# Optimization experiments

Measured on AMD Instinct MI355X. Metric: run time of the kernel, lower is better.

Reference implementation:

```python
import jax, jax.numpy as jnp
import numpy as np

N = 100000   # nodes
E = 1600000  # edges
F = 128      # num_features
H = 128      # hidden width
G = 64       # graphs in batch (target_size)
C = 10       # output_channels


def setup_inputs() -> dict:
    key = jax.random.key(0)
    ks = jax.random.split(key, 16)
    s = 0.05
    inp = {
        "x": jax.random.normal(ks[0], (N, F), jnp.float32),
        "edge_index": jax.random.randint(ks[1], (2, E), 0, N, jnp.int32),
        "batch": jnp.sort(jax.random.randint(ks[2], (N,), 0, G, jnp.int32)),
        "target_size": G,
        # GraphConv layer params: lin_rel (weight+bias) applied to aggregated
        # neighbors, lin_root (weight, no bias) applied to self features.
        "W1_rel": jax.random.normal(ks[3], (H, F), jnp.float32) * s,
        "b1_rel": jnp.zeros((H,), jnp.float32),
        "W1_root": jax.random.normal(ks[4], (H, F), jnp.float32) * s,
        "W2_rel": jax.random.normal(ks[5], (H, H), jnp.float32) * s,
        "b2_rel": jnp.zeros((H,), jnp.float32),
        "W2_root": jax.random.normal(ks[6], (H, H), jnp.float32) * s,
        "W3_rel": jax.random.normal(ks[7], (H, H), jnp.float32) * s,
        "b3_rel": jnp.zeros((H,), jnp.float32),
        "W3_root": jax.random.normal(ks[8], (H, H), jnp.float32) * s,
        "Wl1": jax.random.normal(ks[9], (64, H), jnp.float32) * s,
        "bl1": jnp.zeros((64,), jnp.float32),
        "Wl2": jax.random.normal(ks[10], (C, 64), jnp.float32) * s,
        "bl2": jnp.zeros((C,), jnp.float32),
    }
    return inp


def _graph_conv(x, src, dst, W_rel, b_rel, W_root):
    # PyG GraphConv (aggr='add'): out_i = W_rel @ sum_{j->i} x_j + b_rel + W_root @ x_i
    agg = jax.ops.segment_sum(x[src], dst, num_segments=N)  # [N, F_in]
    return agg @ W_rel.T + b_rel + x @ W_root.T


def reference(x, edge_index, batch, target_size,
              W1_rel, b1_rel, W1_root,
              W2_rel, b2_rel, W2_root,
              W3_rel, b3_rel, W3_root,
              Wl1, bl1, Wl2, bl2):
    src, dst = edge_index[0], edge_index[1]
    h = jax.nn.relu(_graph_conv(x, src, dst, W1_rel, b1_rel, W1_root))
    h = jax.nn.relu(_graph_conv(h, src, dst, W2_rel, b2_rel, W2_root))
    h = jax.nn.relu(_graph_conv(h, src, dst, W3_rel, b3_rel, W3_root))
    # global_mean_pool over graph ids
    sums = jax.ops.segment_sum(h, batch, num_segments=target_size)        # [G, H]
    cnts = jax.ops.segment_sum(jnp.ones((N, 1), h.dtype), batch,
                               num_segments=target_size)                  # [G, 1]
    pooled = sums / jnp.maximum(cnts, 1.0)
    h = jax.nn.relu(pooled @ Wl1.T + bl1)
    return jax.nn.log_softmax(h @ Wl2.T + bl2, axis=-1)
```

## Files before the change

### kernel.cpp

```cpp
#include <hip/hip_runtime.h>

#define N_NODES 100000
#define NPAD    100096
#define N_EDGES 1600000
#define FDIM 128
#define GDIM 64
#define CDIM 10

#define BSH   9
#define BSIZE 512
#define NB    196
#define EPB   8192
#define EPB_C 6250

typedef unsigned short us16;
typedef us16 usx4 __attribute__((ext_vector_type(4)));
typedef us16 usx8 __attribute__((ext_vector_type(8)));
typedef short bfrag __attribute__((ext_vector_type(8)));
typedef float f32x4 __attribute__((ext_vector_type(4)));

__device__ __forceinline__ float bf2f(us16 u) {
  return __uint_as_float(((unsigned)u) << 16);
}
__device__ __forceinline__ us16 f2bf(float f) {
  unsigned u = __float_as_uint(f);
  u += 0x7FFFu + ((u >> 16) & 1u);
  return (us16)(u >> 16);
}

#define XB 6250
__global__ __launch_bounds__(256) void k_prep(
    const float* __restrict__ x, us16* __restrict__ xb,
    const float* __restrict__ Wrel1, const float* __restrict__ Wroot1,
    const float* __restrict__ Wrel2, const float* __restrict__ Wroot2,
    const float* __restrict__ Wrel3, const float* __restrict__ Wroot3,
    us16* __restrict__ Wp, float* __restrict__ pooled,
    const int* __restrict__ edst, int* __restrict__ bcnt) {
  int bx = blockIdx.x, tid = threadIdx.x;
  if (bx < XB) {
    size_t i = ((size_t)bx * 256 + tid) * 8;
    float4 a = *(const float4*)(x + i);
    float4 b = *(const float4*)(x + i + 4);
    usx8 o;
    o[0]=f2bf(a.x); o[1]=f2bf(a.y); o[2]=f2bf(a.z); o[3]=f2bf(a.w);
    o[4]=f2bf(b.x); o[5]=f2bf(b.y); o[6]=f2bf(b.z); o[7]=f2bf(b.w);
    *(usx8*)(xb + i) = o;
  } else if (bx < XB + 384) {
    int wb = bx - XB;
    int l = wb >> 7;
    const float* Wrel  = (l == 0) ? Wrel1  : (l == 1) ? Wrel2  : Wrel3;
    const float* Wroot = (l == 0) ? Wroot1 : (l == 1) ? Wroot2 : Wroot3;
    int idx = (wb & 127) * 256 + tid;
    int k = idx >> 7;
    int c = idx & 127;
    float v = (k < 128) ? Wrel[c * 128 + k] : Wroot[c * 128 + k - 128];
    Wp[(size_t)l * 32768 + (((k >> 3) * 128 + c) << 3) + (k & 7)] = f2bf(v);
  } else if (bx == XB + 384) {
    for (int i = tid; i < GDIM * FDIM; i += 256) pooled[i] = 0.f;
  } else {
    __shared__ int h[NB];
    int cb = bx - (XB + 385);
    for (int i = tid; i < NB; i += 256) h[i] = 0;
    __syncthreads();
    int s0 = cb * EPB;
    int e0 = s0 + EPB; if (e0 > N_EDGES) e0 = N_EDGES;
    for (int i = s0 + tid; i < e0; i += 256) atomicAdd(&h[edst[i] >> BSH], 1);
    __syncthreads();
    for (int i = tid; i < NB; i += 256)
      if (h[i]) atomicAdd(&bcnt[i], h[i]);
  }
}

__device__ __forceinline__ void scan_bcnt(const int* __restrict__ bcnt,
                                          int* wsum ,
                                          int* boffL , int tid) {
  int v = (tid < NB) ? bcnt[tid] : 0;
  int lane = tid & 63;
  int x = v;
#pragma unroll
  for (int d = 1; d < 64; d <<= 1) {
    int t = __shfl_up(x, d, 64);
    if (lane >= d) x += t;
  }
  if (tid < 256 && lane == 63) wsum[tid >> 6] = x;
  __syncthreads();
  if (tid == 0) {
    int r = 0;
#pragma unroll
    for (int i = 0; i < 4; ++i) { int t = wsum[i]; wsum[i] = r; r += t; }
  }
  __syncthreads();
  if (tid < NB) boffL[tid] = x - v + wsum[tid >> 6];
  __syncthreads();
}

__global__ __launch_bounds__(1024) void k_bscatter(
    const int* __restrict__ src, const int* __restrict__ dst,
    const int* __restrict__ bcnt, int* __restrict__ bcursor,
    int* __restrict__ ebuf) {
  __shared__ int wsum[4];
  __shared__ int boffL[NB];
  __shared__ int h[NB];
  __shared__ int base[NB];
  __shared__ int lc[NB];
  int tid = threadIdx.x;
  for (int i = tid; i < NB; i += 1024) h[i] = 0;
  scan_bcnt(bcnt, wsum, boffL, tid);
  int s0 = blockIdx.x * EPB_C;
  int e0 = s0 + EPB_C; if (e0 > N_EDGES) e0 = N_EDGES;
  for (int i = s0 + tid; i < e0; i += 1024) atomicAdd(&h[dst[i] >> BSH], 1);
  __syncthreads();
  for (int i = tid; i < NB; i += 1024) {
    base[i] = h[i] ? (boffL[i] + atomicAdd(&bcursor[i], h[i])) : 0;
    lc[i] = 0;
  }
  __syncthreads();
  for (int i = s0 + tid; i < e0; i += 1024) {
    int d = dst[i];
    int b = d >> BSH;
    int lp = atomicAdd(&lc[b], 1);
    ebuf[base[b] + lp] = (src[i] << BSH) | (d & (BSIZE - 1));
  }
}

__global__ __launch_bounds__(1024) void k_bucket_csr(
    const int* __restrict__ ebuf, const int* __restrict__ bcnt,
    int* __restrict__ row_ptr, int* __restrict__ csr_src) {
  __shared__ int wsum[8];
  __shared__ int boffL[NB];
  __shared__ int hist[BSIZE];
  __shared__ int cur[BSIZE];
  __shared__ int se[2];
  int b = blockIdx.x, tid = threadIdx.x;
  if (tid < BSIZE) hist[tid] = 0;
  scan_bcnt(bcnt, wsum, boffL, tid);
  if (tid == 0) {
    se[0] = boffL[b];
    se[1] = (b + 1 < NB) ? boffL[b + 1] : N_EDGES;
    if (b == 0) row_ptr[N_NODES] = N_EDGES;
  }
  __syncthreads();
  int eoff = se[0], ecnt = se[1] - se[0];
  int base = b * BSIZE;
  for (int i = tid; i < ecnt; i += 1024)
    atomicAdd(&hist[ebuf[eoff + i] & (BSIZE - 1)], 1);
  __syncthreads();
  int v = (tid < BSIZE) ? hist[tid] : 0;
  int lane = tid & 63;
  int x = v;
#pragma unroll
  for (int d = 1; d < 64; d <<= 1) {
    int t = __shfl_up(x, d, 64);
    if (lane >= d) x += t;
  }
  if (tid < BSIZE && lane == 63) wsum[tid >> 6] = x;
  __syncthreads();
  if (tid == 0) {
    int r = 0;
#pragma unroll
    for (int i = 0; i < 8; ++i) { int t = wsum[i]; wsum[i] = r; r += t; }
  }
  __syncthreads();
  if (tid < BSIZE) {
    int ex = x - v + wsum[tid >> 6];
    int node = base + tid;
    if (node < N_NODES) row_ptr[node] = eoff + ex;
    cur[tid] = ex;
  }
  __syncthreads();
  for (int i = tid; i < ecnt; i += 1024) {
    int e = ebuf[eoff + i];
    int lp = atomicAdd(&cur[e & (BSIZE - 1)], 1);
    csr_src[eoff + lp] = e >> BSH;
  }
}

#define ASTR 136
#define LROWS 128
__global__ __launch_bounds__(512) void k_layer(
    const us16* __restrict__ hin, const us16* __restrict__ Wp,
    const float* __restrict__ bias, const int* __restrict__ row_ptr,
    const int* __restrict__ csr_src, us16* __restrict__ out,
    const int* __restrict__ batch, float* __restrict__ pooled) {
  __shared__ us16 As[LROWS * ASTR];
  int tid = threadIdx.x;
  int node0 = blockIdx.x * LROWS;
  int slot = tid >> 4;
  int lane16 = tid & 15;
  const us16* gbase = hin + lane16 * 8;

#pragma unroll 1
  for (int rnd = 0; rnd < 4; ++rnd) {
    int node = node0 + rnd * 32 + slot;
    float a0 = 0.f, a1 = 0.f, a2 = 0.f, a3 = 0.f;
    float a4 = 0.f, a5 = 0.f, a6 = 0.f, a7 = 0.f;
    if (node < N_NODES) {
      int s = row_ptr[node], e = row_ptr[node + 1];
      int p = s;
      for (; p + 4 <= e; p += 4) {
        int j0 = csr_src[p], j1 = csr_src[p + 1];
        int j2 = csr_src[p + 2], j3 = csr_src[p + 3];
        usx8 v0 = *(const usx8*)(gbase + (size_t)j0 * FDIM);
        usx8 v1 = *(const usx8*)(gbase + (size_t)j1 * FDIM);
        usx8 v2 = *(const usx8*)(gbase + (size_t)j2 * FDIM);
        usx8 v3 = *(const usx8*)(gbase + (size_t)j3 * FDIM);
        a0 += bf2f(v0[0]) + bf2f(v1[0]) + bf2f(v2[0]) + bf2f(v3[0]);
        a1 += bf2f(v0[1]) + bf2f(v1[1]) + bf2f(v2[1]) + bf2f(v3[1]);
        a2 += bf2f(v0[2]) + bf2f(v1[2]) + bf2f(v2[2]) + bf2f(v3[2]);
        a3 += bf2f(v0[3]) + bf2f(v1[3]) + bf2f(v2[3]) + bf2f(v3[3]);
        a4 += bf2f(v0[4]) + bf2f(v1[4]) + bf2f(v2[4]) + bf2f(v3[4]);
        a5 += bf2f(v0[5]) + bf2f(v1[5]) + bf2f(v2[5]) + bf2f(v3[5]);
        a6 += bf2f(v0[6]) + bf2f(v1[6]) + bf2f(v2[6]) + bf2f(v3[6]);
        a7 += bf2f(v0[7]) + bf2f(v1[7]) + bf2f(v2[7]) + bf2f(v3[7]);
      }
      for (; p < e; ++p) {
        int j = csr_src[p];
        usx8 v = *(const usx8*)(gbase + (size_t)j * FDIM);
        a0 += bf2f(v[0]); a1 += bf2f(v[1]); a2 += bf2f(v[2]); a3 += bf2f(v[3]);
        a4 += bf2f(v[4]); a5 += bf2f(v[5]); a6 += bf2f(v[6]); a7 += bf2f(v[7]);
      }
    }
    usx8 o;
    o[0] = f2bf(a0); o[1] = f2bf(a1); o[2] = f2bf(a2); o[3] = f2bf(a3);
    o[4] = f2bf(a4); o[5] = f2bf(a5); o[6] = f2bf(a6); o[7] = f2bf(a7);
    *(usx8*)&As[(rnd * 32 + slot) * ASTR + lane16 * 8] = o;
  }
  __syncthreads();

  int wave = tid >> 6, lane = tid & 63;
  int m = lane & 15, quad = lane >> 4;
  size_t rowA = (size_t)(node0 + wave * 16 + m);
  const us16* baseH = hin + rowA * FDIM + quad * 8;
  const us16* aldsb = &As[(wave * 16 + m) * ASTR + quad * 8];
  f32x4 acc[8];
#pragma unroll
  for (int t = 0; t < 8; ++t) acc[t] = (f32x4){0.f, 0.f, 0.f, 0.f};

#pragma unroll 1
  for (int c = 0; c < 8; ++c) {
    bfrag a;
    if (c < 4) a = *(const bfrag*)(aldsb + c * 32);
    else       a = *(const bfrag*)(baseH + (c - 4) * 32);
    int kq = c * 4 + quad;
    const us16* wbase = Wp + (((size_t)kq * 128 + m) << 3);
#pragma unroll
    for (int t = 0; t < 8; ++t) {
      bfrag b = *(const bfrag*)(wbase + t * 128);
      acc[t] = __builtin_amdgcn_mfma_f32_16x16x32_bf16(a, b, acc[t], 0, 0, 0);
    }
  }
  int w16 = node0 + wave * 16;
  int orow0 = w16 + quad * 4;
  if (pooled == nullptr) {
#pragma unroll
    for (int t = 0; t < 8; ++t) {
      int col = t * 16 + m;
      float bv = bias[col];
#pragma unroll
      for (int i = 0; i < 4; ++i) {
        int r = orow0 + i;
        if (r < N_NODES)
          out[(size_t)r * FDIM + col] = f2bf(fmaxf(acc[t][i] + bv, 0.f));
      }
    }
  } else {
    int rlast = w16 + 15;
    int gfirst = batch[(w16 < N_NODES) ? w16 : (N_NODES - 1)];
    int glast  = batch[(rlast < N_NODES) ? rlast : (N_NODES - 1)];
    bool uniform = (gfirst == glast) && (rlast < N_NODES);
    if (uniform) {
#pragma unroll
      for (int t = 0; t < 8; ++t) {
        int col = t * 16 + m;
        float bv = bias[col];
        float v = fmaxf(acc[t][0] + bv, 0.f) + fmaxf(acc[t][1] + bv, 0.f) +
                  fmaxf(acc[t][2] + bv, 0.f) + fmaxf(acc[t][3] + bv, 0.f);
        v += __shfl_xor(v, 16);
        v += __shfl_xor(v, 32);
        if (quad == 0) atomicAdd(&pooled[gfirst * FDIM + col], v);
      }
    } else {
      int g[4];
#pragma unroll
      for (int i = 0; i < 4; ++i) {
        int r = orow0 + i;
        g[i] = batch[(r < N_NODES) ? r : (N_NODES - 1)];
      }
#pragma unroll
      for (int t = 0; t < 8; ++t) {
        int col = t * 16 + m;
        float bv = bias[col];
#pragma unroll
        for (int i = 0; i < 4; ++i) {
          int r = orow0 + i;
          if (r < N_NODES)
            atomicAdd(&pooled[g[i] * FDIM + col], fmaxf(acc[t][i] + bv, 0.f));
        }
      }
    }
  }
}

__global__ __launch_bounds__(128) void k_head(
    const float* __restrict__ pooled, const int* __restrict__ batch,
    const float* __restrict__ Wl1, const float* __restrict__ bl1,
    const float* __restrict__ Wl2, const float* __restrict__ bl2,
    float* __restrict__ out) {
  int g = blockIdx.x;
  __shared__ int sb[2];
  __shared__ float p[128];
  __shared__ float h1[64];
  __shared__ float logit[CDIM];
  if (threadIdx.x < 2) {
    int key = g + (int)threadIdx.x;
    int lo = 0, hi = N_NODES;
    while (lo < hi) {
      int mid = (lo + hi) >> 1;
      if (batch[mid] < key) lo = mid + 1; else hi = mid;
    }
    sb[threadIdx.x] = lo;
  }
  __syncthreads();
  float cnt = (float)(sb[1] - sb[0]);
  p[threadIdx.x] = pooled[g * FDIM + threadIdx.x] / fmaxf(cnt, 1.f);
  __syncthreads();
  if (threadIdx.x < 64) {
    float acc = bl1[threadIdx.x];
    for (int k = 0; k < 128; ++k) acc += p[k] * Wl1[threadIdx.x * 128 + k];
    h1[threadIdx.x] = fmaxf(acc, 0.f);
  }
  __syncthreads();
  if (threadIdx.x < CDIM) {
    float acc = bl2[threadIdx.x];
    for (int k = 0; k < 64; ++k) acc += h1[k] * Wl2[threadIdx.x * 64 + k];
    logit[threadIdx.x] = acc;
  }
  __syncthreads();
  if (threadIdx.x == 0) {
    float m = -1e30f;
    for (int c = 0; c < CDIM; ++c) m = fmaxf(m, logit[c]);
    float s = 0.f;
    for (int c = 0; c < CDIM; ++c) s += expf(logit[c] - m);
    float ls = logf(s);
    for (int c = 0; c < CDIM; ++c) out[g * CDIM + c] = logit[c] - m - ls;
  }
}

extern "C" void kernel_launch(void* const* d_in, const int* in_sizes, int n_in,
                              void* d_out, int out_size, void* d_ws, size_t ws_size,
                              hipStream_t stream) {
  const float* x      = (const float*)d_in[0];
  const int* edge_idx = (const int*)d_in[1];
  const int* batch    = (const int*)d_in[2];
  const float* W1_rel  = (const float*)d_in[4];
  const float* b1_rel  = (const float*)d_in[5];
  const float* W1_root = (const float*)d_in[6];
  const float* W2_rel  = (const float*)d_in[7];
  const float* b2_rel  = (const float*)d_in[8];
  const float* W2_root = (const float*)d_in[9];
  const float* W3_rel  = (const float*)d_in[10];
  const float* b3_rel  = (const float*)d_in[11];
  const float* W3_root = (const float*)d_in[12];
  const float* Wl1     = (const float*)d_in[13];
  const float* bl1     = (const float*)d_in[14];
  const float* Wl2     = (const float*)d_in[15];
  const float* bl2     = (const float*)d_in[16];
  const int* esrc = edge_idx;
  const int* edst = edge_idx + N_EDGES;

  char* ws = (char*)d_ws;
  size_t off = 0;
  auto alloc = [&](size_t bytes) {
    void* p = ws + off;
    off += (bytes + 255) & ~(size_t)255;
    return p;
  };
  int* row_ptr  = (int*)alloc((N_NODES + 1) * sizeof(int));
  int* bc2      = (int*)alloc(2 * NB * sizeof(int));
  int* csr_src  = (int*)alloc(N_EDGES * sizeof(int));
  us16* xb      = (us16*)alloc((size_t)NPAD * FDIM * sizeof(us16));
  us16* hA      = (us16*)alloc((size_t)NPAD * FDIM * sizeof(us16));
  us16* hB      = (us16*)alloc((size_t)NPAD * FDIM * sizeof(us16));
  us16* Wp      = (us16*)alloc(3 * 32768 * sizeof(us16));
  float* pooled = (float*)alloc(GDIM * FDIM * sizeof(float));
  int* bcnt    = bc2;
  int* bcursor = bc2 + NB;
  int* ebuf     = (int*)hA;

  hipMemsetAsync(bc2, 0, 2 * NB * sizeof(int), stream);

  k_prep<<<XB + 384 + 1 + NB, 256, 0, stream>>>(
      x, xb, W1_rel, W1_root, W2_rel, W2_root, W3_rel, W3_root, Wp, pooled,
      edst, bcnt);

  k_bscatter<<<(N_EDGES + EPB_C - 1) / EPB_C, 1024, 0, stream>>>(
      esrc, edst, bcnt, bcursor, ebuf);
  k_bucket_csr<<<NB, 1024, 0, stream>>>(ebuf, bcnt, row_ptr, csr_src);

  int lgrid = NPAD / LROWS;
  k_layer<<<lgrid, 512, 0, stream>>>(xb, Wp,         b1_rel, row_ptr, csr_src,
                                     hA, batch, nullptr);
  k_layer<<<lgrid, 512, 0, stream>>>(hA, Wp + 32768, b2_rel, row_ptr, csr_src,
                                     hB, batch, nullptr);
  k_layer<<<lgrid, 512, 0, stream>>>(hB, Wp + 65536, b3_rel, row_ptr, csr_src,
                                     hA, batch, pooled);

  k_head<<<GDIM, 128, 0, stream>>>(pooled, batch, Wl1, bl1, Wl2, bl2, (float*)d_out);
}
```

Baseline: 427.2 us.

## Split feature matrix into 16-column slices and separate gather from matmul

```diff
diff --git a/kernel.cpp b/kernel.cpp
--- a/kernel.cpp
+++ b/kernel.cpp
@@ -13,8 +13,10 @@
 #define EPB   8192
 #define EPB_C 6250
 
+#define NSLICE 8
+#define SLICE_ELS ((size_t)NPAD * 16)
+
 typedef unsigned short us16;
-typedef us16 usx4 __attribute__((ext_vector_type(4)));
 typedef us16 usx8 __attribute__((ext_vector_type(8)));
 typedef short bfrag __attribute__((ext_vector_type(8)));
 typedef float f32x4 __attribute__((ext_vector_type(4)));
@@ -28,7 +30,7 @@
   return (us16)(u >> 16);
 }
 
-#define XB 6250
+#define CB 6256
 __global__ __launch_bounds__(256) void k_prep(
     const float* __restrict__ x, us16* __restrict__ xb,
     const float* __restrict__ Wrel1, const float* __restrict__ Wroot1,
@@ -37,16 +39,24 @@
     us16* __restrict__ Wp, float* __restrict__ pooled,
     const int* __restrict__ edst, int* __restrict__ bcnt) {
   int bx = blockIdx.x, tid = threadIdx.x;
-  if (bx < XB) {
-    size_t i = ((size_t)bx * 256 + tid) * 8;
-    float4 a = *(const float4*)(x + i);
-    float4 b = *(const float4*)(x + i + 4);
+  if (bx < CB) {
+    int j = bx * 256 + tid;
+    int s = j / (NPAD * 2);
+    int r = j - s * (NPAD * 2);
+    int n = r >> 1, h = r & 1;
     usx8 o;
-    o[0]=f2bf(a.x); o[1]=f2bf(a.y); o[2]=f2bf(a.z); o[3]=f2bf(a.w);
-    o[4]=f2bf(b.x); o[5]=f2bf(b.y); o[6]=f2bf(b.z); o[7]=f2bf(b.w);
-    *(usx8*)(xb + i) = o;
-  } else if (bx < XB + 384) {
-    int wb = bx - XB;
+#pragma unroll
+    for (int k = 0; k < 8; ++k) o[k] = 0;
+    if (n < N_NODES) {
+      const float* xp = x + (size_t)n * FDIM + s * 16 + h * 8;
+      float4 a = *(const float4*)xp;
+      float4 b = *(const float4*)(xp + 4);
+      o[0]=f2bf(a.x); o[1]=f2bf(a.y); o[2]=f2bf(a.z); o[3]=f2bf(a.w);
+      o[4]=f2bf(b.x); o[5]=f2bf(b.y); o[6]=f2bf(b.z); o[7]=f2bf(b.w);
+    }
+    *(usx8*)(xb + (size_t)s * SLICE_ELS + (size_t)n * 16 + h * 8) = o;
+  } else if (bx < CB + 384) {
+    int wb = bx - CB;
     int l = wb >> 7;
     const float* Wrel  = (l == 0) ? Wrel1  : (l == 1) ? Wrel2  : Wrel3;
     const float* Wroot = (l == 0) ? Wroot1 : (l == 1) ? Wroot2 : Wroot3;
@@ -55,11 +65,11 @@
     int c = idx & 127;
     float v = (k < 128) ? Wrel[c * 128 + k] : Wroot[c * 128 + k - 128];
     Wp[(size_t)l * 32768 + (((k >> 3) * 128 + c) << 3) + (k & 7)] = f2bf(v);
-  } else if (bx == XB + 384) {
+  } else if (bx == CB + 384) {
     for (int i = tid; i < GDIM * FDIM; i += 256) pooled[i] = 0.f;
   } else {
     __shared__ int h[NB];
-    int cb = bx - (XB + 385);
+    int cb = bx - (CB + 385);
     for (int i = tid; i < NB; i += 256) h[i] = 0;
     __syncthreads();
     int s0 = cb * EPB;
@@ -175,72 +185,68 @@
   }
 }
 
-#define ASTR 136
+__global__ __launch_bounds__(512) void k_gather(
+    const us16* __restrict__ hin, const int* __restrict__ row_ptr,
+    const int* __restrict__ csr_src, us16* __restrict__ agg) {
+  int slice = blockIdx.x & 7, chunk = blockIdx.x >> 3;
+  int tid = threadIdx.x;
+  int slot = tid >> 1, half = tid & 1;
+  int node = chunk * 256 + slot;
+  const us16* tbl = hin + (size_t)slice * SLICE_ELS + half * 8;
+  float a0=0.f,a1=0.f,a2=0.f,a3=0.f,a4=0.f,a5=0.f,a6=0.f,a7=0.f;
+  if (node < N_NODES) {
+    int s = row_ptr[node], e = row_ptr[node + 1];
+    int p = s;
+    for (; p + 4 <= e; p += 4) {
+      int j0 = csr_src[p],     j1 = csr_src[p + 1];
+      int j2 = csr_src[p + 2], j3 = csr_src[p + 3];
+      usx8 v0 = *(const usx8*)(tbl + (size_t)j0 * 16);
+      usx8 v1 = *(const usx8*)(tbl + (size_t)j1 * 16);
+      usx8 v2 = *(const usx8*)(tbl + (size_t)j2 * 16);
+      usx8 v3 = *(const usx8*)(tbl + (size_t)j3 * 16);
+      a0 += bf2f(v0[0]) + bf2f(v1[0]) + bf2f(v2[0]) + bf2f(v3[0]);
+      a1 += bf2f(v0[1]) + bf2f(v1[1]) + bf2f(v2[1]) + bf2f(v3[1]);
+      a2 += bf2f(v0[2]) + bf2f(v1[2]) + bf2f(v2[2]) + bf2f(v3[2]);
+      a3 += bf2f(v0[3]) + bf2f(v1[3]) + bf2f(v2[3]) + bf2f(v3[3]);
+      a4 += bf2f(v0[4]) + bf2f(v1[4]) + bf2f(v2[4]) + bf2f(v3[4]);
+      a5 += bf2f(v0[5]) + bf2f(v1[5]) + bf2f(v2[5]) + bf2f(v3[5]);
+      a6 += bf2f(v0[6]) + bf2f(v1[6]) + bf2f(v2[6]) + bf2f(v3[6]);
+      a7 += bf2f(v0[7]) + bf2f(v1[7]) + bf2f(v2[7]) + bf2f(v3[7]);
+    }
+    for (; p < e; ++p) {
+      int j = csr_src[p];
+      usx8 v = *(const usx8*)(tbl + (size_t)j * 16);
+      a0 += bf2f(v[0]); a1 += bf2f(v[1]); a2 += bf2f(v[2]); a3 += bf2f(v[3]);
+      a4 += bf2f(v[4]); a5 += bf2f(v[5]); a6 += bf2f(v[6]); a7 += bf2f(v[7]);
+    }
+  }
+  usx8 o;
+  o[0]=f2bf(a0); o[1]=f2bf(a1); o[2]=f2bf(a2); o[3]=f2bf(a3);
+  o[4]=f2bf(a4); o[5]=f2bf(a5); o[6]=f2bf(a6); o[7]=f2bf(a7);
+  *(usx8*)(agg + (size_t)slice * SLICE_ELS + (size_t)node * 16 + half * 8) = o;
+}
+
 #define LROWS 128
-__global__ __launch_bounds__(512) void k_layer(
-    const us16* __restrict__ hin, const us16* __restrict__ Wp,
-    const float* __restrict__ bias, const int* __restrict__ row_ptr,
-    const int* __restrict__ csr_src, us16* __restrict__ out,
-    const int* __restrict__ batch, float* __restrict__ pooled) {
-  __shared__ us16 As[LROWS * ASTR];
+__global__ __launch_bounds__(512) void k_mm(
+    const us16* __restrict__ hin, const us16* __restrict__ agg,
+    const us16* __restrict__ Wp, const float* __restrict__ bias,
+    us16* __restrict__ out, const int* __restrict__ batch,
+    float* __restrict__ pooled) {
   int tid = threadIdx.x;
   int node0 = blockIdx.x * LROWS;
-  int slot = tid >> 4;
-  int lane16 = tid & 15;
-  const us16* gbase = hin + lane16 * 8;
-
-#pragma unroll 1
-  for (int rnd = 0; rnd < 4; ++rnd) {
-    int node = node0 + rnd * 32 + slot;
-    float a0 = 0.f, a1 = 0.f, a2 = 0.f, a3 = 0.f;
-    float a4 = 0.f, a5 = 0.f, a6 = 0.f, a7 = 0.f;
-    if (node < N_NODES) {
-      int s = row_ptr[node], e = row_ptr[node + 1];
-      int p = s;
-      for (; p + 4 <= e; p += 4) {
-        int j0 = csr_src[p], j1 = csr_src[p + 1];
-        int j2 = csr_src[p + 2], j3 = csr_src[p + 3];
-        usx8 v0 = *(const usx8*)(gbase + (size_t)j0 * FDIM);
-        usx8 v1 = *(const usx8*)(gbase + (size_t)j1 * FDIM);
-        usx8 v2 = *(const usx8*)(gbase + (size_t)j2 * FDIM);
-        usx8 v3 = *(const usx8*)(gbase + (size_t)j3 * FDIM);
-        a0 += bf2f(v0[0]) + bf2f(v1[0]) + bf2f(v2[0]) + bf2f(v3[0]);
-        a1 += bf2f(v0[1]) + bf2f(v1[1]) + bf2f(v2[1]) + bf2f(v3[1]);
-        a2 += bf2f(v0[2]) + bf2f(v1[2]) + bf2f(v2[2]) + bf2f(v3[2]);
-        a3 += bf2f(v0[3]) + bf2f(v1[3]) + bf2f(v2[3]) + bf2f(v3[3]);
-        a4 += bf2f(v0[4]) + bf2f(v1[4]) + bf2f(v2[4]) + bf2f(v3[4]);
-        a5 += bf2f(v0[5]) + bf2f(v1[5]) + bf2f(v2[5]) + bf2f(v3[5]);
-        a6 += bf2f(v0[6]) + bf2f(v1[6]) + bf2f(v2[6]) + bf2f(v3[6]);
-        a7 += bf2f(v0[7]) + bf2f(v1[7]) + bf2f(v2[7]) + bf2f(v3[7]);
-      }
-      for (; p < e; ++p) {
-        int j = csr_src[p];
-        usx8 v = *(const usx8*)(gbase + (size_t)j * FDIM);
-        a0 += bf2f(v[0]); a1 += bf2f(v[1]); a2 += bf2f(v[2]); a3 += bf2f(v[3]);
-        a4 += bf2f(v[4]); a5 += bf2f(v[5]); a6 += bf2f(v[6]); a7 += bf2f(v[7]);
-      }
-    }
-    usx8 o;
-    o[0] = f2bf(a0); o[1] = f2bf(a1); o[2] = f2bf(a2); o[3] = f2bf(a3);
-    o[4] = f2bf(a4); o[5] = f2bf(a5); o[6] = f2bf(a6); o[7] = f2bf(a7);
-    *(usx8*)&As[(rnd * 32 + slot) * ASTR + lane16 * 8] = o;
-  }
-  __syncthreads();
-
   int wave = tid >> 6, lane = tid & 63;
   int m = lane & 15, quad = lane >> 4;
   size_t rowA = (size_t)(node0 + wave * 16 + m);
-  const us16* baseH = hin + rowA * FDIM + quad * 8;
-  const us16* aldsb = &As[(wave * 16 + m) * ASTR + quad * 8];
+  int qh = quad >> 1, qo = (quad & 1) * 8;
   f32x4 acc[8];
 #pragma unroll
   for (int t = 0; t < 8; ++t) acc[t] = (f32x4){0.f, 0.f, 0.f, 0.f};
 
 #pragma unroll 1
   for (int c = 0; c < 8; ++c) {
-    bfrag a;
-    if (c < 4) a = *(const bfrag*)(aldsb + c * 32);
-    else       a = *(const bfrag*)(baseH + (c - 4) * 32);
+    const us16* srcb = (c < 4) ? agg : hin;
+    int s = 2 * (c & 3) + qh;
+    bfrag a = *(const bfrag*)(srcb + (size_t)s * SLICE_ELS + rowA * 16 + qo);
     int kq = c * 4 + quad;
     const us16* wbase = Wp + (((size_t)kq * 128 + m) << 3);
 #pragma unroll
@@ -260,7 +266,8 @@
       for (int i = 0; i < 4; ++i) {
         int r = orow0 + i;
         if (r < N_NODES)
-          out[(size_t)r * FDIM + col] = f2bf(fmaxf(acc[t][i] + bv, 0.f));
+          out[(size_t)t * SLICE_ELS + (size_t)r * 16 + m] =
+              f2bf(fmaxf(acc[t][i] + bv, 0.f));
       }
     }
   } else {
@@ -380,7 +387,7 @@
   int* csr_src  = (int*)alloc(N_EDGES * sizeof(int));
   us16* xb      = (us16*)alloc((size_t)NPAD * FDIM * sizeof(us16));
   us16* hA      = (us16*)alloc((size_t)NPAD * FDIM * sizeof(us16));
-  us16* hB      = (us16*)alloc((size_t)NPAD * FDIM * sizeof(us16));
+  us16* agg     = (us16*)alloc((size_t)NPAD * FDIM * sizeof(us16));
   us16* Wp      = (us16*)alloc(3 * 32768 * sizeof(us16));
   float* pooled = (float*)alloc(GDIM * FDIM * sizeof(float));
   int* bcnt    = bc2;
@@ -389,7 +396,7 @@
 
   hipMemsetAsync(bc2, 0, 2 * NB * sizeof(int), stream);
 
-  k_prep<<<XB + 384 + 1 + NB, 256, 0, stream>>>(
+  k_prep<<<CB + 384 + 1 + NB, 256, 0, stream>>>(
       x, xb, W1_rel, W1_root, W2_rel, W2_root, W3_rel, W3_root, Wp, pooled,
       edst, bcnt);
 
@@ -397,13 +404,15 @@
       esrc, edst, bcnt, bcursor, ebuf);
   k_bucket_csr<<<NB, 1024, 0, stream>>>(ebuf, bcnt, row_ptr, csr_src);
 
-  int lgrid = NPAD / LROWS;
-  k_layer<<<lgrid, 512, 0, stream>>>(xb, Wp,         b1_rel, row_ptr, csr_src,
-                                     hA, batch, nullptr);
-  k_layer<<<lgrid, 512, 0, stream>>>(hA, Wp + 32768, b2_rel, row_ptr, csr_src,
-                                     hB, batch, nullptr);
-  k_layer<<<lgrid, 512, 0, stream>>>(hB, Wp + 65536, b3_rel, row_ptr, csr_src,
-                                     hA, batch, pooled);
+  int ggrid = (NPAD / 256) * NSLICE;
+  int mgrid = NPAD / LROWS;
+
+  k_gather<<<ggrid, 512, 0, stream>>>(xb, row_ptr, csr_src, agg);
+  k_mm<<<mgrid, 512, 0, stream>>>(xb, agg, Wp, b1_rel, hA, batch, nullptr);
+  k_gather<<<ggrid, 512, 0, stream>>>(hA, row_ptr, csr_src, agg);
+  k_mm<<<mgrid, 512, 0, stream>>>(hA, agg, Wp + 32768, b2_rel, xb, batch, nullptr);
+  k_gather<<<ggrid, 512, 0, stream>>>(xb, row_ptr, csr_src, agg);
+  k_mm<<<mgrid, 512, 0, stream>>>(xb, agg, Wp + 65536, b3_rel, hA, batch, pooled);
 
   k_head<<<GDIM, 128, 0, stream>>>(pooled, batch, Wl1, bl1, Wl2, bl2, (float*)d_out);
 }
```

New measurement: 528.8 us. 23.8% more time.

## Gather neighbor features from FP8 copies to halve aggregation traffic

Applied to the files above, without the earlier changes.

```diff
diff --git a/kernel.cpp b/kernel.cpp
--- a/kernel.cpp
+++ b/kernel.cpp
@@ -14,10 +14,11 @@
 #define EPB_C 6250
 
 typedef unsigned short us16;
-typedef us16 usx4 __attribute__((ext_vector_type(4)));
+typedef unsigned char u8;
 typedef us16 usx8 __attribute__((ext_vector_type(8)));
 typedef short bfrag __attribute__((ext_vector_type(8)));
 typedef float f32x4 __attribute__((ext_vector_type(4)));
+typedef float f32x2 __attribute__((ext_vector_type(2)));
 
 __device__ __forceinline__ float bf2f(us16 u) {
   return __uint_as_float(((unsigned)u) << 16);
@@ -28,9 +29,18 @@
   return (us16)(u >> 16);
 }
 
+__device__ __forceinline__ void acc_fp8x8(uint2 v, float* a) {
+  f32x2 p0 = __builtin_amdgcn_cvt_pk_f32_fp8(v.x, false);
+  f32x2 p1 = __builtin_amdgcn_cvt_pk_f32_fp8(v.x, true);
+  f32x2 p2 = __builtin_amdgcn_cvt_pk_f32_fp8(v.y, false);
+  f32x2 p3 = __builtin_amdgcn_cvt_pk_f32_fp8(v.y, true);
+  a[0] += p0[0]; a[1] += p0[1]; a[2] += p1[0]; a[3] += p1[1];
+  a[4] += p2[0]; a[5] += p2[1]; a[6] += p3[0]; a[7] += p3[1];
+}
+
 #define XB 6250
 __global__ __launch_bounds__(256) void k_prep(
-    const float* __restrict__ x, us16* __restrict__ xb,
+    const float* __restrict__ x, us16* __restrict__ xb, u8* __restrict__ xq,
     const float* __restrict__ Wrel1, const float* __restrict__ Wroot1,
     const float* __restrict__ Wrel2, const float* __restrict__ Wroot2,
     const float* __restrict__ Wrel3, const float* __restrict__ Wroot3,
@@ -45,6 +55,12 @@
     o[0]=f2bf(a.x); o[1]=f2bf(a.y); o[2]=f2bf(a.z); o[3]=f2bf(a.w);
     o[4]=f2bf(b.x); o[5]=f2bf(b.y); o[6]=f2bf(b.z); o[7]=f2bf(b.w);
     *(usx8*)(xb + i) = o;
+    int lo = __builtin_amdgcn_cvt_pk_fp8_f32(a.x, a.y, 0, false);
+    lo     = __builtin_amdgcn_cvt_pk_fp8_f32(a.z, a.w, lo, true);
+    int hi = __builtin_amdgcn_cvt_pk_fp8_f32(b.x, b.y, 0, false);
+    hi     = __builtin_amdgcn_cvt_pk_fp8_f32(b.z, b.w, hi, true);
+    uint2 q; q.x = (unsigned)lo; q.y = (unsigned)hi;
+    *(uint2*)(xq + i) = q;
   } else if (bx < XB + 384) {
     int wb = bx - XB;
     int l = wb >> 7;
@@ -178,51 +194,46 @@
 #define ASTR 136
 #define LROWS 128
 __global__ __launch_bounds__(512) void k_layer(
-    const us16* __restrict__ hin, const us16* __restrict__ Wp,
-    const float* __restrict__ bias, const int* __restrict__ row_ptr,
-    const int* __restrict__ csr_src, us16* __restrict__ out,
+    const us16* __restrict__ hin, const u8* __restrict__ hq_in,
+    const us16* __restrict__ Wp, const float* __restrict__ bias,
+    const int* __restrict__ row_ptr, const int* __restrict__ csr_src,
+    us16* __restrict__ out, u8* __restrict__ hq_out,
     const int* __restrict__ batch, float* __restrict__ pooled) {
   __shared__ us16 As[LROWS * ASTR];
   int tid = threadIdx.x;
   int node0 = blockIdx.x * LROWS;
   int slot = tid >> 4;
   int lane16 = tid & 15;
-  const us16* gbase = hin + lane16 * 8;
+  const u8* gbase = hq_in + lane16 * 8;
 
 #pragma unroll 1
   for (int rnd = 0; rnd < 4; ++rnd) {
     int node = node0 + rnd * 32 + slot;
-    float a0 = 0.f, a1 = 0.f, a2 = 0.f, a3 = 0.f;
-    float a4 = 0.f, a5 = 0.f, a6 = 0.f, a7 = 0.f;
+    float a[8];
+#pragma unroll
+    for (int j = 0; j < 8; ++j) a[j] = 0.f;
     if (node < N_NODES) {
       int s = row_ptr[node], e = row_ptr[node + 1];
       int p = s;
       for (; p + 4 <= e; p += 4) {
         int j0 = csr_src[p], j1 = csr_src[p + 1];
         int j2 = csr_src[p + 2], j3 = csr_src[p + 3];
-        usx8 v0 = *(const usx8*)(gbase + (size_t)j0 * FDIM);
-        usx8 v1 = *(const usx8*)(gbase + (size_t)j1 * FDIM);
-        usx8 v2 = *(const usx8*)(gbase + (size_t)j2 * FDIM);
-        usx8 v3 = *(const usx8*)(gbase + (size_t)j3 * FDIM);
-        a0 += bf2f(v0[0]) + bf2f(v1[0]) + bf2f(v2[0]) + bf2f(v3[0]);
-        a1 += bf2f(v0[1]) + bf2f(v1[1]) + bf2f(v2[1]) + bf2f(v3[1]);
-        a2 += bf2f(v0[2]) + bf2f(v1[2]) + bf2f(v2[2]) + bf2f(v3[2]);
-        a3 += bf2f(v0[3]) + bf2f(v1[3]) + bf2f(v2[3]) + bf2f(v3[3]);
-        a4 += bf2f(v0[4]) + bf2f(v1[4]) + bf2f(v2[4]) + bf2f(v3[4]);
-        a5 += bf2f(v0[5]) + bf2f(v1[5]) + bf2f(v2[5]) + bf2f(v3[5]);
-        a6 += bf2f(v0[6]) + bf2f(v1[6]) + bf2f(v2[6]) + bf2f(v3[6]);
-        a7 += bf2f(v0[7]) + bf2f(v1[7]) + bf2f(v2[7]) + bf2f(v3[7]);
+        uint2 v0 = *(const uint2*)(gbase + (size_t)j0 * FDIM);
+        uint2 v1 = *(const uint2*)(gbase + (size_t)j1 * FDIM);
+        uint2 v2 = *(const uint2*)(gbase + (size_t)j2 * FDIM);
+        uint2 v3 = *(const uint2*)(gbase + (size_t)j3 * FDIM);
+        acc_fp8x8(v0, a); acc_fp8x8(v1, a);
+        acc_fp8x8(v2, a); acc_fp8x8(v3, a);
       }
       for (; p < e; ++p) {
         int j = csr_src[p];
-        usx8 v = *(const usx8*)(gbase + (size_t)j * FDIM);
-        a0 += bf2f(v[0]); a1 += bf2f(v[1]); a2 += bf2f(v[2]); a3 += bf2f(v[3]);
-        a4 += bf2f(v[4]); a5 += bf2f(v[5]); a6 += bf2f(v[6]); a7 += bf2f(v[7]);
+        uint2 v = *(const uint2*)(gbase + (size_t)j * FDIM);
+        acc_fp8x8(v, a);
       }
     }
     usx8 o;
-    o[0] = f2bf(a0); o[1] = f2bf(a1); o[2] = f2bf(a2); o[3] = f2bf(a3);
-    o[4] = f2bf(a4); o[5] = f2bf(a5); o[6] = f2bf(a6); o[7] = f2bf(a7);
+#pragma unroll
+    for (int j = 0; j < 8; ++j) o[j] = f2bf(a[j]);
     *(usx8*)&As[(rnd * 32 + slot) * ASTR + lane16 * 8] = o;
   }
   __syncthreads();
@@ -259,8 +270,12 @@
 #pragma unroll
       for (int i = 0; i < 4; ++i) {
         int r = orow0 + i;
-        if (r < N_NODES)
-          out[(size_t)r * FDIM + col] = f2bf(fmaxf(acc[t][i] + bv, 0.f));
+        if (r < N_NODES) {
+          float val = fmaxf(acc[t][i] + bv, 0.f);
+          out[(size_t)r * FDIM + col] = f2bf(val);
+          hq_out[(size_t)r * FDIM + col] =
+              (u8)(__builtin_amdgcn_cvt_pk_fp8_f32(val, val, 0, false) & 0xFF);
+        }
       }
     }
   } else {
@@ -380,7 +395,8 @@
   int* csr_src  = (int*)alloc(N_EDGES * sizeof(int));
   us16* xb      = (us16*)alloc((size_t)NPAD * FDIM * sizeof(us16));
   us16* hA      = (us16*)alloc((size_t)NPAD * FDIM * sizeof(us16));
-  us16* hB      = (us16*)alloc((size_t)NPAD * FDIM * sizeof(us16));
+  u8*   xq      = (u8*)alloc((size_t)NPAD * FDIM);
+  u8*   hqA     = (u8*)alloc((size_t)NPAD * FDIM);
   us16* Wp      = (us16*)alloc(3 * 32768 * sizeof(us16));
   float* pooled = (float*)alloc(GDIM * FDIM * sizeof(float));
   int* bcnt    = bc2;
@@ -390,7 +406,7 @@
   hipMemsetAsync(bc2, 0, 2 * NB * sizeof(int), stream);
 
   k_prep<<<XB + 384 + 1 + NB, 256, 0, stream>>>(
-      x, xb, W1_rel, W1_root, W2_rel, W2_root, W3_rel, W3_root, Wp, pooled,
+      x, xb, xq, W1_rel, W1_root, W2_rel, W2_root, W3_rel, W3_root, Wp, pooled,
       edst, bcnt);
 
   k_bscatter<<<(N_EDGES + EPB_C - 1) / EPB_C, 1024, 0, stream>>>(
@@ -398,12 +414,12 @@
   k_bucket_csr<<<NB, 1024, 0, stream>>>(ebuf, bcnt, row_ptr, csr_src);
 
   int lgrid = NPAD / LROWS;
-  k_layer<<<lgrid, 512, 0, stream>>>(xb, Wp,         b1_rel, row_ptr, csr_src,
-                                     hA, batch, nullptr);
-  k_layer<<<lgrid, 512, 0, stream>>>(hA, Wp + 32768, b2_rel, row_ptr, csr_src,
-                                     hB, batch, nullptr);
-  k_layer<<<lgrid, 512, 0, stream>>>(hB, Wp + 65536, b3_rel, row_ptr, csr_src,
-                                     hA, batch, pooled);
+  k_layer<<<lgrid, 512, 0, stream>>>(xb, xq, Wp, b1_rel, row_ptr, csr_src,
+                                     hA, hqA, batch, nullptr);
+  k_layer<<<lgrid, 512, 0, stream>>>(hA, hqA, Wp + 32768, b2_rel, row_ptr,
+                                     csr_src, xb, xq, batch, nullptr);
+  k_layer<<<lgrid, 512, 0, stream>>>(xb, xq, Wp + 65536, b3_rel, row_ptr,
+                                     csr_src, hA, nullptr, batch, pooled);
 
   k_head<<<GDIM, 128, 0, stream>>>(pooled, batch, Wl1, bl1, Wl2, bl2, (float*)d_out);
 }
```

Result: faster. 375.8 us (-12.0%).
